# Performance work log

Measured on AMD Instinct MI355X. Metric: run time of the kernel, lower is better.

Reference implementation:

```python
import jax, jax.numpy as jnp
import numpy as np


def setup_inputs() -> dict:
    key = jax.random.key(0)
    doc_embeddings = jax.random.normal(key, (16384, 128), dtype=jnp.float32)
    return {"doc_embeddings": doc_embeddings}


def reference(doc_embeddings) -> jnp.ndarray:
    n = doc_embeddings.shape[0]
    # [N, N] pairwise dot products
    scores = jnp.matmul(doc_embeddings, doc_embeddings.T)
    positive_scores = jnp.diagonal(scores)  # [N]
    # zero out the diagonal (matches dot - eye*dot in the torch code)
    diag_mask = jnp.eye(n, dtype=scores.dtype)
    negative_scores = scores - diag_mask * scores
    positive_loss = jax.nn.log_sigmoid(positive_scores)            # [N]
    negative_loss = jax.nn.log_sigmoid(-negative_scores).sum(axis=1)  # [N]
    loss = -(positive_loss + negative_loss).mean()
    return loss
```

## Files before the change

### kernel.cpp

```cpp
#include <hip/hip_runtime.h>
#include <hip/hip_bf16.h>


#define N_DOCS 16384
#define DIM 128
#define NTILE 128
#define NTRI (NTILE * (NTILE + 1) / 2)
#define PBLOCKS 768

typedef __attribute__((ext_vector_type(4))) float f32x4;
typedef __attribute__((ext_vector_type(8))) __bf16 bf16x8;
typedef __attribute__((ext_vector_type(2))) long longx2;

typedef const __attribute__((address_space(1))) unsigned char* gptr_t;
typedef __attribute__((address_space(3))) unsigned char* lptr_t;

#define SQRT_LOG2E 1.2011224087864498f
#define LN2F 0.6931471805599453f
#define QC0 1.33985f
#define QC1 (-0.33985f)

#if __has_builtin(__builtin_amdgcn_exp2f)
#define EXP2F(x) __builtin_amdgcn_exp2f(x)
#else
#define EXP2F(x) exp2f(x)
#endif

#define BARRIER() do { asm volatile("" ::: "memory"); \
                       __builtin_amdgcn_s_barrier();  \
                       asm volatile("" ::: "memory"); } while (0)

__device__ __forceinline__ unsigned short f2bf(float f) {
  unsigned int u = __float_as_uint(f);
  u += 0x7fffu + ((u >> 16) & 1u);
  return (unsigned short)(u >> 16);
}

#if __has_builtin(__builtin_amdgcn_cvt_pk_fp8_f32)
#define HAVE_CVT_FP8 1
#else
__device__ __forceinline__ unsigned char f2e4m3(float x) {
  unsigned int u = __float_as_uint(x);
  unsigned char sgn = (unsigned char)((u >> 31) << 7);
  float ax = fabsf(x);
  if (!(ax < 464.f)) return sgn | 0x7E;
  unsigned int ua = u & 0x7FFFFFFFu;
  int e = (int)(ua >> 23) - 127;
  if (e < -6) {
    float q = rintf(ax * 512.f);
    return sgn | (unsigned char)q;
  }
  unsigned int mant = ua & 0x7FFFFFu;
  unsigned int keep = mant >> 20;
  unsigned int rest = mant & 0xFFFFFu;
  keep += (rest > 0x80000u) || (rest == 0x80000u && (keep & 1u));
  unsigned int ee = (unsigned int)(e + 7);
  if (keep == 8u) { keep = 0u; ee++; }
  if (ee >= 16u) return sgn | 0x7E;
  return sgn | (unsigned char)((ee << 3) | keep);
}
#endif

__device__ __forceinline__ void tri_decode(int g, int& tr, int& tc) {
  int r = (int)((2 * NTILE + 1 -
                 sqrtf((float)((2 * NTILE + 1) * (2 * NTILE + 1)) - 8.0f * (float)g)) * 0.5f);
  while (r * NTILE - r * (r - 1) / 2 > g) --r;
  while ((r + 1) * NTILE - (r + 1) * r / 2 <= g) ++r;
  tr = r;
  tc = r + (g - (r * NTILE - r * (r - 1) / 2));
}

__global__ __launch_bounds__(256) void cast_kernel(const float* __restrict__ in,
                                                   unsigned char* __restrict__ out,
                                                   float* __restrict__ rpart,
                                                   float* __restrict__ colpart) {
  __shared__ float cs[16][136];
  __shared__ float redr[4];
  const int b = blockIdx.x, tid = threadIdx.x;
  const int kb = tid & 15, rg = tid >> 4;

  float csum[8] = {0.f, 0.f, 0.f, 0.f, 0.f, 0.f, 0.f, 0.f};
  float rsum = 0.f;
#pragma unroll
  for (int it = 0; it < 8; ++it) {
    int r = it * 16 + rg;
    int row = b * 128 + r;
    const float4* p = reinterpret_cast<const float4*>(in + (size_t)row * 128 + kb * 8);
    float4 a = p[0], c = p[1];
    float v0 = a.x * SQRT_LOG2E, v1 = a.y * SQRT_LOG2E, v2 = a.z * SQRT_LOG2E,
          v3 = a.w * SQRT_LOG2E, v4 = c.x * SQRT_LOG2E, v5 = c.y * SQRT_LOG2E,
          v6 = c.z * SQRT_LOG2E, v7 = c.w * SQRT_LOG2E;
    int w0, w1;
#ifdef HAVE_CVT_FP8
    w0 = __builtin_amdgcn_cvt_pk_fp8_f32(v0, v1, 0, false);
    w0 = __builtin_amdgcn_cvt_pk_fp8_f32(v2, v3, w0, true);
    w1 = __builtin_amdgcn_cvt_pk_fp8_f32(v4, v5, 0, false);
    w1 = __builtin_amdgcn_cvt_pk_fp8_f32(v6, v7, w1, true);
#else
    w0 = (int)f2e4m3(v0) | ((int)f2e4m3(v1) << 8) | ((int)f2e4m3(v2) << 16) | ((int)f2e4m3(v3) << 24);
    w1 = (int)f2e4m3(v4) | ((int)f2e4m3(v5) << 8) | ((int)f2e4m3(v6) << 16) | ((int)f2e4m3(v7) << 24);
#endif
    int g = kb & 3, s = kb >> 2;
    int off = b * 16384 + (g * 2 + (s >> 1)) * 2048 + r * 16 + (s & 1) * 8;
    *reinterpret_cast<int2*>(out + off) = make_int2(w0, w1);
    csum[0] += v0; csum[1] += v1; csum[2] += v2; csum[3] += v3;
    csum[4] += v4; csum[5] += v5; csum[6] += v6; csum[7] += v7;
    rsum = fmaf(v0, v0, rsum); rsum = fmaf(v1, v1, rsum);
    rsum = fmaf(v2, v2, rsum); rsum = fmaf(v3, v3, rsum);
    rsum = fmaf(v4, v4, rsum); rsum = fmaf(v5, v5, rsum);
    rsum = fmaf(v6, v6, rsum); rsum = fmaf(v7, v7, rsum);
  }
#pragma unroll
  for (int j = 0; j < 8; ++j) cs[rg][kb * 8 + j] = csum[j];
#pragma unroll
  for (int off = 32; off > 0; off >>= 1) rsum += __shfl_down(rsum, off);
  if ((tid & 63) == 0) redr[tid >> 6] = rsum;
  __syncthreads();
  if (tid < 128) {
    float s = 0.f;
#pragma unroll
    for (int r = 0; r < 16; ++r) s += cs[r][tid];
    colpart[b * 128 + tid] = s;
  }
  if (tid == 0) rpart[b] = redr[0] + redr[1] + redr[2] + redr[3];
}

__global__ __launch_bounds__(512, 6) void loss_persist(const unsigned char* __restrict__ ef8,
                                                       float* __restrict__ accum,
                                                       unsigned int* __restrict__ counter,
                                                       const float* __restrict__ rpart,
                                                       const float* __restrict__ colpart,
                                                       float* __restrict__ out) {
  __shared__ alignas(16) unsigned char Asl[16384];
  __shared__ alignas(16) unsigned char Bsl[2][16384];
  __shared__ float red[8];
  __shared__ int lastFlag;
  const int tid = threadIdx.x;
  const int p = blockIdx.x;
  const int g0 = (p * 43) >> 2;
  const int g1 = ((p + 1) * 43) >> 2;
  const int n = g1 - g0;

  const int wid = tid >> 6;
  const int lane = tid & 63;
  const int wm = wid >> 2, wn = wid & 3;
  const int lrow = lane & 15;
  const int kgrp = lane >> 4;

  auto stageA = [&](int t) {
    const unsigned char* s = ef8 + (size_t)t * 16384;
#pragma unroll
    for (int it = 0; it < 2; ++it) {
      int pp = (it * 512 + tid) * 16;
      __builtin_amdgcn_global_load_lds((gptr_t)(s + pp), (lptr_t)(Asl + pp), 16, 0, 0);
    }
  };
  auto stageB = [&](int t, int buf) {
    const unsigned char* s = ef8 + (size_t)t * 16384;
#pragma unroll
    for (int it = 0; it < 2; ++it) {
      int pp = (it * 512 + tid) * 16;
      __builtin_amdgcn_global_load_lds((gptr_t)(s + pp), (lptr_t)(Bsl[buf] + pp), 16, 0, 0);
    }
  };

  auto compute = [&](int buf) -> float {
    const unsigned char* As = (const unsigned char*)Asl;
    const unsigned char* Bs = (const unsigned char*)Bsl[buf];

    f32x4 acc[4][2];
#pragma unroll
    for (int a = 0; a < 4; ++a)
#pragma unroll
      for (int c = 0; c < 2; ++c) acc[a][c] = (f32x4){0.f, 0.f, 0.f, 0.f};

#pragma unroll
    for (int ks2 = 0; ks2 < 2; ++ks2) {
      longx2 af[4], bf[2];
      const int pbase = (kgrp * 2 + ks2) * 2048;
#pragma unroll
      for (int f = 0; f < 4; ++f) {
        int ar = wm * 64 + f * 16 + lrow;
        af[f] = *reinterpret_cast<const longx2*>(As + pbase + ar * 16);
      }
#pragma unroll
      for (int f = 0; f < 2; ++f) {
        int br = wn * 32 + f * 16 + lrow;
        bf[f] = *reinterpret_cast<const longx2*>(Bs + pbase + br * 16);
      }
#pragma unroll
      for (int fm = 0; fm < 4; ++fm)
#pragma unroll
        for (int fn = 0; fn < 2; ++fn) {
          acc[fm][fn] = __builtin_amdgcn_mfma_f32_16x16x32_fp8_fp8(af[fm].x, bf[fn].x,
                                                                   acc[fm][fn], 0, 0, 0);
          acc[fm][fn] = __builtin_amdgcn_mfma_f32_16x16x32_fp8_fp8(af[fm].y, bf[fn].y,
                                                                   acc[fm][fn], 0, 0, 0);
        }
    }

    float sa = 0.f, su = 0.f;
#pragma unroll
    for (int fm = 0; fm < 4; ++fm)
#pragma unroll
      for (int fn = 0; fn < 2; ++fn)
#pragma unroll
        for (int r = 0; r < 4; ++r) {
          float a = fabsf(acc[fm][fn][r]);
          sa += a;
          float u = EXP2F(-a);
          su = fmaf(u, fmaf(u, QC1, QC0), su);
        }
    return fmaf(0.5f, sa, su);
  };

  int tr, tc;
  tri_decode(g0, tr, tc);
  float total = 0.f;
  int buf = 0;
  stageA(tr);
  stageB(tc, 0);
  for (int i = 0; i < n; ++i) {
    int ntr = tr, ntc = tc + 1;
    if (ntc == NTILE) { ntr = tr + 1; ntc = ntr; }
    const bool have_next = (i + 1 < n);
    const bool samerow = have_next && (ntr == tr);
    if (samerow) {
      stageB(ntc, buf ^ 1);
      asm volatile("s_waitcnt vmcnt(2)" ::: "memory");
    } else {
      asm volatile("s_waitcnt vmcnt(0)" ::: "memory");
    }
    BARRIER();
    total += (tr == tc ? 1.f : 2.f) * compute(buf);
    BARRIER();
    if (have_next && !samerow) {
      stageA(ntr);
      stageB(ntc, buf ^ 1);
    }
    tr = ntr; tc = ntc; buf ^= 1;
  }

#pragma unroll
  for (int off = 32; off > 0; off >>= 1) total += __shfl_down(total, off);
  if (lane == 0) red[wid] = total;
  __syncthreads();
  if (tid == 0) {
    float t = red[0] + red[1] + red[2] + red[3] + red[4] + red[5] + red[6] + red[7];
    atomicAdd(accum, t);
    __threadfence();
    unsigned int old = atomicAdd(counter, 1u);
    lastFlag = (old == (unsigned int)(PBLOCKS - 1));
  }
  __syncthreads();
  if (lastFlag) {
    float part = 0.f;
    if (tid < 128) {
      float cs = 0.f;
#pragma unroll 8
      for (int b = 0; b < 128; ++b) cs += colpart[b * 128 + tid];
      part = fmaf(0.5f * cs, cs, -rpart[tid]);
    }
    if (tid < 128) {
#pragma unroll
      for (int off = 32; off > 0; off >>= 1) part += __shfl_down(part, off);
      if (lane == 0) red[wid] = part;
    }
    __syncthreads();
    if (tid == 0) {
      float tail = red[0] + red[1];
      float acc = atomicAdd(accum, 0.f);
      out[0] = LN2F * ((acc + tail) * (1.0f / (float)N_DOCS) + 1.0f);
    }
  }
}

__global__ __launch_bounds__(512, 2) void loss_fallback(const float* __restrict__ src,
                                                        float* __restrict__ accum) {
  const int b = blockIdx.x;
  int tr, tc;
  tri_decode(b, tr, tc);

  __shared__ alignas(16) unsigned short As[128 * 128];
  __shared__ alignas(16) unsigned short Bs[128 * 128];
  __shared__ float red[8];
  const int tid = threadIdx.x;

  const float4* srcA4 = (const float4*)(src + (size_t)tr * 16384);
  const float4* srcB4 = (const float4*)(src + (size_t)tc * 16384);
#pragma unroll
  for (int it = 0; it < 8; ++it) {
    int idx = it * 512 + tid;
    int L = idx * 8;
    int swz = L ^ (((L >> 8) & 7) << 4);
    float4 a = srcA4[idx];
    ushort4 oa = {f2bf(a.x * SQRT_LOG2E), f2bf(a.y * SQRT_LOG2E),
                  f2bf(a.z * SQRT_LOG2E), f2bf(a.w * SQRT_LOG2E)};
    *reinterpret_cast<ushort4*>((unsigned char*)As + swz) = oa;
    float4 bb = srcB4[idx];
    ushort4 ob = {f2bf(bb.x * SQRT_LOG2E), f2bf(bb.y * SQRT_LOG2E),
                  f2bf(bb.z * SQRT_LOG2E), f2bf(bb.w * SQRT_LOG2E)};
    *reinterpret_cast<ushort4*>((unsigned char*)Bs + swz) = ob;
  }
  __syncthreads();

  const int wid = tid >> 6;
  const int lane = tid & 63;
  const int wm = wid >> 2, wn = wid & 3;
  const int lrow = lane & 15;
  const int kgrp = lane >> 4;

  f32x4 acc[4][2];
#pragma unroll
  for (int a = 0; a < 4; ++a)
#pragma unroll
    for (int c = 0; c < 2; ++c) acc[a][c] = (f32x4){0.f, 0.f, 0.f, 0.f};

#pragma unroll
  for (int ks = 0; ks < 4; ++ks) {
    bf16x8 af[4], bfr[2];
#pragma unroll
    for (int f = 0; f < 4; ++f) {
      int ar = wm * 64 + f * 16 + lrow;
      int ab = (ar * 256 + ks * 64 + kgrp * 16) ^ ((ar & 7) << 4);
      af[f] = *reinterpret_cast<const bf16x8*>((const unsigned char*)As + ab);
    }
#pragma unroll
    for (int f = 0; f < 2; ++f) {
      int br = wn * 32 + f * 16 + lrow;
      int bb = (br * 256 + ks * 64 + kgrp * 16) ^ ((br & 7) << 4);
      bfr[f] = *reinterpret_cast<const bf16x8*>((const unsigned char*)Bs + bb);
    }
#pragma unroll
    for (int fm = 0; fm < 4; ++fm)
#pragma unroll
      for (int fn = 0; fn < 2; ++fn)
        acc[fm][fn] = __builtin_amdgcn_mfma_f32_16x16x32_bf16(af[fm], bfr[fn], acc[fm][fn], 0, 0, 0);
  }

  float sm = 0.f, sp = 0.f;
  if (tr == tc) {
#pragma unroll
    for (int fm = 0; fm < 4; ++fm)
#pragma unroll
      for (int fn = 0; fn < 2; ++fn)
#pragma unroll
        for (int r = 0; r < 4; ++r) {
          float v = acc[fm][fn][r];
          int il = wm * 64 + fm * 16 + kgrp * 4 + r;
          int jl = wn * 32 + fn * 16 + lrow;
          if (il == jl) v = -v;
          sm += fmaxf(v, 0.f);
          float u = EXP2F(-fabsf(v));
          sp = fmaf(u, fmaf(u, QC1, QC0), sp);
        }
  } else {
#pragma unroll
    for (int fm = 0; fm < 4; ++fm)
#pragma unroll
      for (int fn = 0; fn < 2; ++fn)
#pragma unroll
        for (int r = 0; r < 4; ++r) {
          float v = acc[fm][fn][r];
          sm += fmaxf(v, 0.f);
          float u = EXP2F(-fabsf(v));
          sp = fmaf(u, fmaf(u, QC1, QC0), sp);
        }
    sm *= 2.f;
    sp *= 2.f;
  }

  float lsum = sm + sp;
#pragma unroll
  for (int off = 32; off > 0; off >>= 1) lsum += __shfl_down(lsum, off);
  if (lane == 0) red[wid] = lsum;
  __syncthreads();
  if (tid == 0) {
    float t = red[0] + red[1] + red[2] + red[3] + red[4] + red[5] + red[6] + red[7];
    atomicAdd(accum, t);
  }
}

__global__ void finalize_kernel(const float* __restrict__ accum, float* __restrict__ out) {
  out[0] = LN2F * (accum[0] * (1.0f / (float)N_DOCS) + 1.0f);
}

extern "C" void kernel_launch(void* const* d_in, const int* in_sizes, int n_in,
                              void* d_out, int out_size, void* d_ws, size_t ws_size,
                              hipStream_t stream) {
  const float* E = (const float*)d_in[0];
  float* out = (float*)d_out;
  float* accum = (float*)d_ws;
  unsigned int* counter = (unsigned int*)((char*)d_ws + 64);
  float* rpart = (float*)((char*)d_ws + 256);
  float* colpart = (float*)((char*)d_ws + 1024);
  unsigned char* ef8 = (unsigned char*)d_ws + 66560;

  const size_t need = 66560 + (size_t)N_DOCS * DIM + 256;
  if (ws_size >= need) {
    (void)hipMemsetAsync(d_ws, 0, 256, stream);
    cast_kernel<<<128, 256, 0, stream>>>(E, ef8, rpart, colpart);
    loss_persist<<<PBLOCKS, 512, 0, stream>>>(ef8, accum, counter, rpart, colpart, out);
  } else {
    (void)hipMemsetAsync(accum, 0, sizeof(float), stream);
    loss_fallback<<<NTRI, 512, 0, stream>>>(E, accum);
    finalize_kernel<<<1, 1, 0, stream>>>(accum, out);
  }
}
```

Baseline: 106.0 us.

## Use MX-scaled 16x16x128 fp8 MFMA, raise wave priority, fold memset into cast

When the compiler exposes the gfx950 scaled MFMA builtin, each wave covers the full 128-wide K slice with one 16x16x128 fp8 instruction per output fragment, using neutral scales, in place of four 16x16x32 instructions. Wave priority is raised around the MFMA bursts so matrix work gets issue preference. The host-side memset of the accumulator and counter is dropped, and cast_kernel block 0 zeroes them instead, saving one launch. This relies on the accumulator being visible as zero before the persistent kernel's atomics run, which the in-stream launch order provides.

```diff
diff --git a/kernel.cpp b/kernel.cpp
--- a/kernel.cpp
+++ b/kernel.cpp
@@ -24,6 +24,11 @@
 #define EXP2F(x) __builtin_amdgcn_exp2f(x)
 #else
 #define EXP2F(x) exp2f(x)
+#endif
+
+#if __has_builtin(__builtin_amdgcn_mfma_scale_f32_16x16x128_f8f6f4)
+#define HAVE_MX 1
+typedef __attribute__((ext_vector_type(8))) int i32x8;
 #endif
 
 #define BARRIER() do { asm volatile("" ::: "memory"); \
@@ -73,11 +78,14 @@
 __global__ __launch_bounds__(256) void cast_kernel(const float* __restrict__ in,
                                                    unsigned char* __restrict__ out,
                                                    float* __restrict__ rpart,
-                                                   float* __restrict__ colpart) {
+                                                   float* __restrict__ colpart,
+                                                   float* __restrict__ accum,
+                                                   unsigned int* __restrict__ counter) {
   __shared__ float cs[16][136];
   __shared__ float redr[4];
   const int b = blockIdx.x, tid = threadIdx.x;
   const int kb = tid & 15, rg = tid >> 4;
+  if (b == 0 && tid == 0) { accum[0] = 0.f; *counter = 0u; }
 
   float csum[8] = {0.f, 0.f, 0.f, 0.f, 0.f, 0.f, 0.f, 0.f};
   float rsum = 0.f;
@@ -174,6 +182,30 @@
 #pragma unroll
       for (int c = 0; c < 2; ++c) acc[a][c] = (f32x4){0.f, 0.f, 0.f, 0.f};
 
+#ifdef HAVE_MX
+    const int pbase = kgrp * 2 * 2048;
+    i32x8 b8[2];
+#pragma unroll
+    for (int f = 0; f < 2; ++f) {
+      int br = wn * 32 + f * 16 + lrow;
+      int4 lo = *reinterpret_cast<const int4*>(Bs + pbase + br * 16);
+      int4 hi = *reinterpret_cast<const int4*>(Bs + pbase + 2048 + br * 16);
+      b8[f] = (i32x8){lo.x, lo.y, lo.z, lo.w, hi.x, hi.y, hi.z, hi.w};
+    }
+    __builtin_amdgcn_s_setprio(1);
+#pragma unroll
+    for (int fm = 0; fm < 4; ++fm) {
+      int ar = wm * 64 + fm * 16 + lrow;
+      int4 lo = *reinterpret_cast<const int4*>(As + pbase + ar * 16);
+      int4 hi = *reinterpret_cast<const int4*>(As + pbase + 2048 + ar * 16);
+      i32x8 a8 = (i32x8){lo.x, lo.y, lo.z, lo.w, hi.x, hi.y, hi.z, hi.w};
+#pragma unroll
+      for (int fn = 0; fn < 2; ++fn)
+        acc[fm][fn] = __builtin_amdgcn_mfma_scale_f32_16x16x128_f8f6f4(
+            a8, b8[fn], acc[fm][fn], 0, 0, 0, 127, 0, 127);
+    }
+    __builtin_amdgcn_s_setprio(0);
+#else
 #pragma unroll
     for (int ks2 = 0; ks2 < 2; ++ks2) {
       longx2 af[4], bf[2];
@@ -188,6 +220,7 @@
         int br = wn * 32 + f * 16 + lrow;
         bf[f] = *reinterpret_cast<const longx2*>(Bs + pbase + br * 16);
       }
+      __builtin_amdgcn_s_setprio(1);
 #pragma unroll
       for (int fm = 0; fm < 4; ++fm)
 #pragma unroll
@@ -197,7 +230,9 @@
           acc[fm][fn] = __builtin_amdgcn_mfma_f32_16x16x32_fp8_fp8(af[fm].y, bf[fn].y,
                                                                    acc[fm][fn], 0, 0, 0);
         }
-    }
+      __builtin_amdgcn_s_setprio(0);
+    }
+#endif
 
     float sa = 0.f, su = 0.f;
 #pragma unroll
@@ -260,8 +295,6 @@
 #pragma unroll 8
       for (int b = 0; b < 128; ++b) cs += colpart[b * 128 + tid];
       part = fmaf(0.5f * cs, cs, -rpart[tid]);
-    }
-    if (tid < 128) {
 #pragma unroll
       for (int off = 32; off > 0; off >>= 1) part += __shfl_down(part, off);
       if (lane == 0) red[wid] = part;
@@ -398,8 +431,7 @@
 
   const size_t need = 66560 + (size_t)N_DOCS * DIM + 256;
   if (ws_size >= need) {
-    (void)hipMemsetAsync(d_ws, 0, 256, stream);
-    cast_kernel<<<128, 256, 0, stream>>>(E, ef8, rpart, colpart);
+    cast_kernel<<<128, 256, 0, stream>>>(E, ef8, rpart, colpart, accum, counter);
     loss_persist<<<PBLOCKS, 512, 0, stream>>>(ef8, accum, counter, rpart, colpart, out);
   } else {
     (void)hipMemsetAsync(accum, 0, sizeof(float), stream);
```

Result: faster. 100.8 us (-4.9%).
